# Kernel tuning notes

Hardware: AMD Instinct MI355X
Metric: run time of the kernel (lower is better)

## Reference

```python
import jax, jax.numpy as jnp
import numpy as np


def setup_inputs() -> dict:
    key = jax.random.key(0)
    k1, k2 = jax.random.split(key)
    B, V = 8192, 32000
    outputs = jax.random.normal(k1, (B, V), dtype=jnp.float32)
    targets = jax.random.randint(k2, (B,), 0, V, dtype=jnp.int64)
    return {"outputs": outputs, "targets": targets}


def reference(outputs, targets):
    # stable log-softmax over vocab, then gather target log-prob per row
    logp = jax.nn.log_softmax(outputs, axis=-1)          # [B, V]
    picked = jnp.take_along_axis(logp, targets[:, None], axis=-1)[:, 0]  # [B]
    return -jnp.mean(picked)
```

## Files before the change

kernel.cpp:

```cpp
#include <hip/hip_runtime.h>
#include <math.h>


#define LOG2E 1.4426950408889634f
#define LN2   0.6931471805599453f

__global__ __launch_bounds__(256) void ce_row_kernel(const float* __restrict__ x,
                                                     const int* __restrict__ tgt,
                                                     float* __restrict__ row_loss,
                                                     int V, int B) {
    const int wave = threadIdx.x >> 6;
    const int lane = threadIdx.x & 63;
    const int row  = (blockIdx.x << 2) + wave;
    if (row >= B) return;

    const float* __restrict__ xr = x + (size_t)row * (size_t)V;
    const float4* __restrict__ xv = (const float4*)xr;
    const int nvec = V >> 2;

    float m0 = -INFINITY, m1 = -INFINITY, m2 = -INFINITY, m3 = -INFINITY;
    float s0 = 0.f, s1 = 0.f, s2 = 0.f, s3 = 0.f;

    #pragma unroll 5
    for (int i = lane; i < nvec; i += 64) {
        float4 v = xv[i];
        float w0 = v.x * LOG2E, w1 = v.y * LOG2E,
              w2 = v.z * LOG2E, w3 = v.w * LOG2E;
        float n0 = fmaxf(m0, w0);
        s0 = s0 * exp2f(m0 - n0) + exp2f(w0 - n0); m0 = n0;
        float n1 = fmaxf(m1, w1);
        s1 = s1 * exp2f(m1 - n1) + exp2f(w1 - n1); m1 = n1;
        float n2 = fmaxf(m2, w2);
        s2 = s2 * exp2f(m2 - n2) + exp2f(w2 - n2); m2 = n2;
        float n3 = fmaxf(m3, w3);
        s3 = s3 * exp2f(m3 - n3) + exp2f(w3 - n3); m3 = n3;
    }

    float M = fmaxf(fmaxf(m0, m1), fmaxf(m2, m3));
    float S = s0 * exp2f(m0 - M) + s1 * exp2f(m1 - M)
            + s2 * exp2f(m2 - M) + s3 * exp2f(m3 - M);

    #pragma unroll
    for (int off = 1; off < 64; off <<= 1) {
        float om = __shfl_xor(M, off);
        float os = __shfl_xor(S, off);
        float mn = fmaxf(M, om);
        S = S * exp2f(M - mn) + os * exp2f(om - mn);
        M = mn;
    }

    if (lane == 0) {
        float lse = (M + log2f(S)) * LN2;
        row_loss[row] = lse - xr[tgt[row]];
    }
}

__global__ __launch_bounds__(256) void ce_reduce_kernel(const float* __restrict__ row_loss,
                                                        float* __restrict__ out, int B) {
    float acc = 0.0f;
    for (int i = threadIdx.x; i < B; i += 256) acc += row_loss[i];
    #pragma unroll
    for (int off = 1; off < 64; off <<= 1) acc += __shfl_xor(acc, off);
    __shared__ float sa[4];
    if ((threadIdx.x & 63) == 0) sa[threadIdx.x >> 6] = acc;
    __syncthreads();
    if (threadIdx.x == 0) out[0] = (sa[0] + sa[1] + sa[2] + sa[3]) / (float)B;
}

extern "C" void kernel_launch(void* const* d_in, const int* in_sizes, int n_in,
                              void* d_out, int out_size, void* d_ws, size_t ws_size,
                              hipStream_t stream) {
    const float* x = (const float*)d_in[0];
    const int* tgt = (const int*)d_in[1];
    float* out = (float*)d_out;
    float* ws = (float*)d_ws;

    const int B = in_sizes[1];
    const int V = in_sizes[0] / B;

    ce_row_kernel<<<(B + 3) / 4, 256, 0, stream>>>(x, tgt, ws, V, B);
    ce_reduce_kernel<<<1, 256, 0, stream>>>(ws, out, B);
}
```

Before: 201.4 us.

## Process one row per 256-thread block with nontemporal loads

Each row is now handled by a whole 256-thread block instead of a single wave. The four per-wave partial max/sum pairs are combined through shared memory and one barrier. Input loads use nontemporal hints, since the 1 GB logits tensor is streamed once. This gives each row more parallelism and spreads the work over 8192 blocks, at the cost of a shared-memory combine and a sync per row, and the unroll pragma is removed.

```diff
diff --git a/kernel.cpp b/kernel.cpp
--- a/kernel.cpp
+++ b/kernel.cpp
@@ -5,25 +5,24 @@
 #define LOG2E 1.4426950408889634f
 #define LN2   0.6931471805599453f
 
+typedef float floatx4 __attribute__((ext_vector_type(4)));
+
 __global__ __launch_bounds__(256) void ce_row_kernel(const float* __restrict__ x,
                                                      const int* __restrict__ tgt,
                                                      float* __restrict__ row_loss,
-                                                     int V, int B) {
-    const int wave = threadIdx.x >> 6;
-    const int lane = threadIdx.x & 63;
-    const int row  = (blockIdx.x << 2) + wave;
-    if (row >= B) return;
+                                                     int V) {
+    const int row = blockIdx.x;
+    const float* __restrict__ xr = x + (size_t)row * (size_t)V;
+    const int tid = threadIdx.x;
 
-    const float* __restrict__ xr = x + (size_t)row * (size_t)V;
-    const float4* __restrict__ xv = (const float4*)xr;
     const int nvec = V >> 2;
+    const floatx4* __restrict__ xv = (const floatx4*)xr;
 
     float m0 = -INFINITY, m1 = -INFINITY, m2 = -INFINITY, m3 = -INFINITY;
     float s0 = 0.f, s1 = 0.f, s2 = 0.f, s3 = 0.f;
 
-    #pragma unroll 5
-    for (int i = lane; i < nvec; i += 64) {
-        float4 v = xv[i];
+    for (int i = tid; i < nvec; i += 256) {
+        floatx4 v = __builtin_nontemporal_load(&xv[i]);
         float w0 = v.x * LOG2E, w1 = v.y * LOG2E,
               w2 = v.z * LOG2E, w3 = v.w * LOG2E;
         float n0 = fmaxf(m0, w0);
@@ -49,8 +48,21 @@
         M = mn;
     }
 
-    if (lane == 0) {
-        float lse = (M + log2f(S)) * LN2;
+    __shared__ float sm[4], ss[4];
+    const int wave = tid >> 6;
+    if ((tid & 63) == 0) { sm[wave] = M; ss[wave] = S; }
+    __syncthreads();
+
+    if (tid == 0) {
+        float Mf = sm[0], Sf = ss[0];
+        #pragma unroll
+        for (int w = 1; w < 4; ++w) {
+            float om = sm[w], os = ss[w];
+            float mn = fmaxf(Mf, om);
+            Sf = Sf * exp2f(Mf - mn) + os * exp2f(om - mn);
+            Mf = mn;
+        }
+        float lse = (Mf + log2f(Sf)) * LN2;
         row_loss[row] = lse - xr[tgt[row]];
     }
 }
@@ -78,6 +90,6 @@
     const int B = in_sizes[1];
     const int V = in_sizes[0] / B;
 
-    ce_row_kernel<<<(B + 3) / 4, 256, 0, stream>>>(x, tgt, ws, V, B);
+    ce_row_kernel<<<B, 256, 0, stream>>>(x, tgt, ws, V);
     ce_reduce_kernel<<<1, 256, 0, stream>>>(ws, out, B);
 }
```

Result: faster. 176.2 us (-12.5%).
